# Kernel optimization log

Measured on AMD Instinct MI355X. Metric: run time of the kernel, lower is better.

The kernel has to match this reference:

```python
import jax, jax.numpy as jnp
import numpy as np


def setup_inputs() -> dict:
    key = jax.random.key(0)
    k1, k2 = jax.random.split(key)
    B, N, P = 8, 16384, 2048
    xyz = jax.random.uniform(k1, (B, N, 3), dtype=jnp.float32)
    center_xyz = jax.random.uniform(k2, (B, P, 3), dtype=jnp.float32)
    return {
        "xyz": xyz,
        "center_xyz": center_xyz,
        "max_radius": jnp.float32(0.2),
        "sample_num": 32,
    }


def reference(xyz, center_xyz, max_radius, sample_num):
    # xyz: [B, N, 3], center_xyz: [B, P, 3] -> idx: [B, P, sample_num] int32
    B, P, _ = center_xyz.shape
    N = xyz.shape[1]
    S = int(sample_num)

    # squared distances via ||c||^2 + ||x||^2 - 2 c.x (avoids [B,P,N,3] temp)
    xn = jnp.sum(xyz * xyz, axis=-1)                      # [B, N]
    cn = jnp.sum(center_xyz * center_xyz, axis=-1)        # [B, P]
    dot = jnp.einsum("bpd,bnd->bpn", center_xyz, xyz)     # [B, P, N]
    d2 = cn[:, :, None] + xn[:, None, :] - 2.0 * dot       # [B, P, N]

    mask = d2 < (max_radius * max_radius)                  # dist < r  <=>  dist^2 < r^2
    # rank of each point among the valid ones (in index order), as in torch.where order
    rank = jnp.cumsum(mask.astype(jnp.int32), axis=-1) - 1 # [B, P, N]
    take = mask & (rank < S)
    # valid points write into slot=rank; everything else into dump slot S (discarded)
    slot = jnp.where(take, rank, S)                        # [B, P, N]

    buf = jnp.zeros((B, P, S + 1), dtype=jnp.int32)        # zeros match torch init fill
    bi = jnp.arange(B)[:, None, None]
    pi = jnp.arange(P)[None, :, None]
    src = jnp.broadcast_to(jnp.arange(N, dtype=jnp.int32), (B, P, N))
    buf = buf.at[bi, pi, slot].set(src)
    return buf[:, :, :S]
```

## Files before the change

kernel.cpp:

```cpp
#include <hip/hip_runtime.h>
#include <hip/hip_bf16.h>


typedef float f32x4 __attribute__((ext_vector_type(4)));

__global__ __launch_bounds__(256) void pack_points(
    const float* __restrict__ xyz,
    f32x4* __restrict__ q,
    int total)
{
    const int n = blockIdx.x * blockDim.x + threadIdx.x;
    if (n >= total) return;
    const float x = xyz[(size_t)n * 3 + 0];
    const float y = xyz[(size_t)n * 3 + 1];
    const float z = xyz[(size_t)n * 3 + 2];
    const float xn = __builtin_fmaf(z, z,
                      __builtin_fmaf(y, y, __fmul_rn(x, x)));
    f32x4 v;
    v[0] = x; v[1] = y; v[2] = z; v[3] = xn;
    q[n] = v;
}

__global__ __launch_bounds__(64) void ball_query_wave4(
    const f32x4* __restrict__ q,
    const float* __restrict__ center,
    const float* __restrict__ p_radius,
    const int*   __restrict__ p_sample,
    int* __restrict__ out,
    int B, int N, int P)
{
    const int S = p_sample[0];
    const float r = p_radius[0];
    const float r2 = __fmul_rn(r, r);

    const int b = blockIdx.x & 7;
    const int g = blockIdx.x >> 3;
    const int c0 = b * P + g * 4;
    const int lane = threadIdx.x;

    float cx[4], cy[4], cz[4], cn[4];
    int cnt[4];
#pragma unroll
    for (int i = 0; i < 4; ++i) {
        const size_t c = (size_t)(c0 + i);
        cx[i] = center[c * 3 + 0];
        cy[i] = center[c * 3 + 1];
        cz[i] = center[c * 3 + 2];
        cn[i] = __builtin_fmaf(cz[i], cz[i],
                 __builtin_fmaf(cy[i], cy[i], __fmul_rn(cx[i], cx[i])));
        cnt[i] = 0;
    }

    const f32x4* qb = q + (size_t)b * N;
    int* ob = out + (size_t)c0 * S;

    for (int n0 = 0; n0 < N; n0 += 512) {
        if (cnt[0] >= S && cnt[1] >= S && cnt[2] >= S && cnt[3] >= S) break;

        f32x4 v[8];
#pragma unroll
        for (int j = 0; j < 8; ++j) {
            v[j] = qb[n0 + j * 64 + lane];
        }

#pragma unroll
        for (int i = 0; i < 4; ++i) {
            if (cnt[i] >= S) continue;
            int cc = cnt[i];
#pragma unroll
            for (int j = 0; j < 8; ++j) {
                const float x = v[j][0], y = v[j][1], z = v[j][2];
                const float xn = v[j][3];
                const float dot = __builtin_fmaf(cz[i], z,
                                   __builtin_fmaf(cy[i], y, __fmul_rn(cx[i], x)));
                const float d2 = __fsub_rn(__fadd_rn(cn[i], xn),
                                           __fmul_rn(2.0f, dot));

                const bool valid = d2 < r2;
                const unsigned long long m = __ballot(valid);
                const int rank = __builtin_amdgcn_mbcnt_hi(
                    (unsigned)(m >> 32),
                    __builtin_amdgcn_mbcnt_lo((unsigned)m, 0u));
                if (valid && (cc + rank) < S) {
                    ob[i * S + cc + rank] = n0 + j * 64 + lane;
                }
                cc += __popcll(m);
            }
            cnt[i] = cc;
        }
    }

#pragma unroll
    for (int i = 0; i < 4; ++i) {
        int c = cnt[i] > S ? S : cnt[i];
        for (int s = c + lane; s < S; s += 64) {
            ob[i * S + s] = 0;
        }
    }
}

extern "C" void kernel_launch(void* const* d_in, const int* in_sizes, int n_in,
                              void* d_out, int out_size, void* d_ws, size_t ws_size,
                              hipStream_t stream) {
    const float* xyz      = (const float*)d_in[0];
    const float* center   = (const float*)d_in[1];
    const float* p_radius = (const float*)d_in[2];
    const int*   p_sample = (const int*)d_in[3];

    const int B = 8;
    const int N = in_sizes[0] / (B * 3);
    const int P = in_sizes[1] / (B * 3);

    int* out = (int*)d_out;
    f32x4* q = (f32x4*)d_ws;

    const int total = B * N;
    pack_points<<<(total + 255) / 256, 256, 0, stream>>>(xyz, q, total);

    const int blocks = B * (P / 4);
    ball_query_wave4<<<blocks, 64, 0, stream>>>(
        q, center, p_radius, p_sample, out, B, N, P);
}
```

Measured before the change: 78.17 us.

## Use planar point layout with packed fp32 math and batched ballots

```diff
diff --git a/kernel.cpp b/kernel.cpp
--- a/kernel.cpp
+++ b/kernel.cpp
@@ -1,12 +1,35 @@
 #include <hip/hip_runtime.h>
-#include <hip/hip_bf16.h>
 
 
 typedef float f32x4 __attribute__((ext_vector_type(4)));
-
-__global__ __launch_bounds__(256) void pack_points(
+typedef float f32x2 __attribute__((ext_vector_type(2)));
+
+__device__ __forceinline__ f32x2 pk_mul(f32x2 a, f32x2 b) {
+    f32x2 d;
+    asm("v_pk_mul_f32 %0, %1, %2" : "=v"(d) : "v"(a), "v"(b));
+    return d;
+}
+__device__ __forceinline__ f32x2 pk_fma(f32x2 a, f32x2 b, f32x2 c) {
+    f32x2 d;
+    asm("v_pk_fma_f32 %0, %1, %2, %3" : "=v"(d) : "v"(a), "v"(b), "v"(c));
+    return d;
+}
+__device__ __forceinline__ f32x2 pk_add(f32x2 a, f32x2 b) {
+    f32x2 d;
+    asm("v_pk_add_f32 %0, %1, %2" : "=v"(d) : "v"(a), "v"(b));
+    return d;
+}
+__device__ __forceinline__ f32x2 pk_sub(f32x2 a, f32x2 b) {
+    f32x2 d;
+    asm("v_pk_add_f32 %0, %1, %2 neg_lo:[0,1] neg_hi:[0,1]"
+        : "=v"(d) : "v"(a), "v"(b));
+    return d;
+}
+
+__global__ __launch_bounds__(256) void pack_planes(
     const float* __restrict__ xyz,
-    f32x4* __restrict__ q,
+    float* __restrict__ qx, float* __restrict__ qy,
+    float* __restrict__ qz, float* __restrict__ qw,
     int total)
 {
     const int n = blockIdx.x * blockDim.x + threadIdx.x;
@@ -16,13 +39,67 @@
     const float z = xyz[(size_t)n * 3 + 2];
     const float xn = __builtin_fmaf(z, z,
                       __builtin_fmaf(y, y, __fmul_rn(x, x)));
-    f32x4 v;
-    v[0] = x; v[1] = y; v[2] = z; v[3] = xn;
-    q[n] = v;
-}
-
-__global__ __launch_bounds__(64) void ball_query_wave4(
-    const f32x4* __restrict__ q,
+    qx[n] = x; qy[n] = y; qz[n] = z; qw[n] = xn;
+}
+
+__device__ __forceinline__ int process_group(
+    f32x2 xlo, f32x2 xhi, f32x2 ylo, f32x2 yhi,
+    f32x2 zlo, f32x2 zhi, f32x2 wlo, f32x2 whi,
+    int vbase,
+    f32x2 pcx, f32x2 pcy, f32x2 pcz, f32x2 pcn, f32x2 p2,
+    int cc, int* __restrict__ obi, int S, float r2)
+{
+    f32x2 t0 = pk_mul(pcx, xlo);
+    t0 = pk_fma(pcy, ylo, t0);
+    t0 = pk_fma(pcz, zlo, t0);
+    f32x2 t1 = pk_mul(pcx, xhi);
+    t1 = pk_fma(pcy, yhi, t1);
+    t1 = pk_fma(pcz, zhi, t1);
+    f32x2 a0 = pk_add(pcn, wlo);
+    f32x2 a1 = pk_add(pcn, whi);
+    f32x2 b0 = pk_mul(p2, t0);
+    f32x2 b1 = pk_mul(p2, t1);
+    f32x2 d0 = pk_sub(a0, b0);
+    f32x2 d1 = pk_sub(a1, b1);
+
+    const bool v0 = d0[0] < r2;
+    const bool v1 = d0[1] < r2;
+    const bool v2 = d1[0] < r2;
+    const bool v3 = d1[1] < r2;
+    const unsigned long long m0 = __ballot(v0);
+    const unsigned long long m1 = __ballot(v1);
+    const unsigned long long m2 = __ballot(v2);
+    const unsigned long long m3 = __ballot(v3);
+
+    if ((m0 | m1 | m2 | m3) == 0ull) return cc;
+
+    int R = __builtin_amdgcn_mbcnt_lo((unsigned)m0, 0u);
+    R = __builtin_amdgcn_mbcnt_hi((unsigned)(m0 >> 32), R);
+    R = __builtin_amdgcn_mbcnt_lo((unsigned)m1, R);
+    R = __builtin_amdgcn_mbcnt_hi((unsigned)(m1 >> 32), R);
+    R = __builtin_amdgcn_mbcnt_lo((unsigned)m2, R);
+    R = __builtin_amdgcn_mbcnt_hi((unsigned)(m2 >> 32), R);
+    R = __builtin_amdgcn_mbcnt_lo((unsigned)m3, R);
+    R = __builtin_amdgcn_mbcnt_hi((unsigned)(m3 >> 32), R);
+
+    const int rank0 = R;
+    const int rank1 = rank0 + (v0 ? 1 : 0);
+    const int rank2 = rank1 + (v1 ? 1 : 0);
+    const int rank3 = rank2 + (v2 ? 1 : 0);
+
+    const int lim = S - cc;
+    if (v0 && rank0 < lim) obi[cc + rank0] = vbase + 0;
+    if (v1 && rank1 < lim) obi[cc + rank1] = vbase + 1;
+    if (v2 && rank2 < lim) obi[cc + rank2] = vbase + 2;
+    if (v3 && rank3 < lim) obi[cc + rank3] = vbase + 3;
+
+    cc += __popcll(m0) + __popcll(m1) + __popcll(m2) + __popcll(m3);
+    return cc;
+}
+
+__global__ __launch_bounds__(64) void ball_query_pk(
+    const float* __restrict__ qx, const float* __restrict__ qy,
+    const float* __restrict__ qz, const float* __restrict__ qw,
     const float* __restrict__ center,
     const float* __restrict__ p_radius,
     const int*   __restrict__ p_sample,
@@ -38,53 +115,64 @@
     const int c0 = b * P + g * 4;
     const int lane = threadIdx.x;
 
-    float cx[4], cy[4], cz[4], cn[4];
+    f32x2 pcx[4], pcy[4], pcz[4], pcn[4];
     int cnt[4];
 #pragma unroll
     for (int i = 0; i < 4; ++i) {
         const size_t c = (size_t)(c0 + i);
-        cx[i] = center[c * 3 + 0];
-        cy[i] = center[c * 3 + 1];
-        cz[i] = center[c * 3 + 2];
-        cn[i] = __builtin_fmaf(cz[i], cz[i],
-                 __builtin_fmaf(cy[i], cy[i], __fmul_rn(cx[i], cx[i])));
+        const float cx = center[c * 3 + 0];
+        const float cy = center[c * 3 + 1];
+        const float cz = center[c * 3 + 2];
+        const float cn = __builtin_fmaf(cz, cz,
+                          __builtin_fmaf(cy, cy, __fmul_rn(cx, cx)));
+        pcx[i][0] = cx; pcx[i][1] = cx;
+        pcy[i][0] = cy; pcy[i][1] = cy;
+        pcz[i][0] = cz; pcz[i][1] = cz;
+        pcn[i][0] = cn; pcn[i][1] = cn;
         cnt[i] = 0;
     }
-
-    const f32x4* qb = q + (size_t)b * N;
+    f32x2 p2; p2[0] = 2.0f; p2[1] = 2.0f;
+
+    const f32x4* X4 = (const f32x4*)(qx + (size_t)b * N);
+    const f32x4* Y4 = (const f32x4*)(qy + (size_t)b * N);
+    const f32x4* Z4 = (const f32x4*)(qz + (size_t)b * N);
+    const f32x4* W4 = (const f32x4*)(qw + (size_t)b * N);
     int* ob = out + (size_t)c0 * S;
 
     for (int n0 = 0; n0 < N; n0 += 512) {
         if (cnt[0] >= S && cnt[1] >= S && cnt[2] >= S && cnt[3] >= S) break;
 
-        f32x4 v[8];
-#pragma unroll
-        for (int j = 0; j < 8; ++j) {
-            v[j] = qb[n0 + j * 64 + lane];
-        }
+        const int i0 = (n0 >> 2) + lane;
+        const f32x4 xv0 = X4[i0],      yv0 = Y4[i0];
+        const f32x4 zv0 = Z4[i0],      wv0 = W4[i0];
+        const f32x4 xv1 = X4[i0 + 64], yv1 = Y4[i0 + 64];
+        const f32x4 zv1 = Z4[i0 + 64], wv1 = W4[i0 + 64];
+
+        f32x2 x0l, x0h, y0l, y0h, z0l, z0h, w0l, w0h;
+        f32x2 x1l, x1h, y1l, y1h, z1l, z1h, w1l, w1h;
+        x0l[0]=xv0[0]; x0l[1]=xv0[1]; x0h[0]=xv0[2]; x0h[1]=xv0[3];
+        y0l[0]=yv0[0]; y0l[1]=yv0[1]; y0h[0]=yv0[2]; y0h[1]=yv0[3];
+        z0l[0]=zv0[0]; z0l[1]=zv0[1]; z0h[0]=zv0[2]; z0h[1]=zv0[3];
+        w0l[0]=wv0[0]; w0l[1]=wv0[1]; w0h[0]=wv0[2]; w0h[1]=wv0[3];
+        x1l[0]=xv1[0]; x1l[1]=xv1[1]; x1h[0]=xv1[2]; x1h[1]=xv1[3];
+        y1l[0]=yv1[0]; y1l[1]=yv1[1]; y1h[0]=yv1[2]; y1h[1]=yv1[3];
+        z1l[0]=zv1[0]; z1l[1]=zv1[1]; z1h[0]=zv1[2]; z1h[1]=zv1[3];
+        w1l[0]=wv1[0]; w1l[1]=wv1[1]; w1h[0]=wv1[2]; w1h[1]=wv1[3];
+
+        const int vbase0 = n0 + 4 * lane;
+        const int vbase1 = vbase0 + 256;
 
 #pragma unroll
         for (int i = 0; i < 4; ++i) {
             if (cnt[i] >= S) continue;
             int cc = cnt[i];
-#pragma unroll
-            for (int j = 0; j < 8; ++j) {
-                const float x = v[j][0], y = v[j][1], z = v[j][2];
-                const float xn = v[j][3];
-                const float dot = __builtin_fmaf(cz[i], z,
-                                   __builtin_fmaf(cy[i], y, __fmul_rn(cx[i], x)));
-                const float d2 = __fsub_rn(__fadd_rn(cn[i], xn),
-                                           __fmul_rn(2.0f, dot));
-
-                const bool valid = d2 < r2;
-                const unsigned long long m = __ballot(valid);
-                const int rank = __builtin_amdgcn_mbcnt_hi(
-                    (unsigned)(m >> 32),
-                    __builtin_amdgcn_mbcnt_lo((unsigned)m, 0u));
-                if (valid && (cc + rank) < S) {
-                    ob[i * S + cc + rank] = n0 + j * 64 + lane;
-                }
-                cc += __popcll(m);
+            cc = process_group(x0l, x0h, y0l, y0h, z0l, z0h, w0l, w0h,
+                               vbase0, pcx[i], pcy[i], pcz[i], pcn[i], p2,
+                               cc, ob + i * S, S, r2);
+            if (cc < S) {
+                cc = process_group(x1l, x1h, y1l, y1h, z1l, z1h, w1l, w1h,
+                                   vbase1, pcx[i], pcy[i], pcz[i], pcn[i], p2,
+                                   cc, ob + i * S, S, r2);
             }
             cnt[i] = cc;
         }
@@ -112,12 +200,17 @@
     const int P = in_sizes[1] / (B * 3);
 
     int* out = (int*)d_out;
-    f32x4* q = (f32x4*)d_ws;
-
     const int total = B * N;
-    pack_points<<<(total + 255) / 256, 256, 0, stream>>>(xyz, q, total);
+
+    float* qx = (float*)d_ws;
+    float* qy = qx + total;
+    float* qz = qy + total;
+    float* qw = qz + total;
+
+    pack_planes<<<(total + 255) / 256, 256, 0, stream>>>(
+        xyz, qx, qy, qz, qw, total);
 
     const int blocks = B * (P / 4);
-    ball_query_wave4<<<blocks, 64, 0, stream>>>(
-        q, center, p_radius, p_sample, out, B, N, P);
-}
+    ball_query_pk<<<blocks, 64, 0, stream>>>(
+        qx, qy, qz, qw, center, p_radius, p_sample, out, B, N, P);
+}
```

Result: no change. 78.47 us (+0.4%).

## Fuse point packing into ball query and process four contiguous points per lane

Applied to the files above, without the earlier changes.

```diff
diff --git a/kernel.cpp b/kernel.cpp
--- a/kernel.cpp
+++ b/kernel.cpp
@@ -1,28 +1,67 @@
 #include <hip/hip_runtime.h>
-#include <hip/hip_bf16.h>
 
 
 typedef float f32x4 __attribute__((ext_vector_type(4)));
 
-__global__ __launch_bounds__(256) void pack_points(
-    const float* __restrict__ xyz,
-    f32x4* __restrict__ q,
-    int total)
+__device__ __forceinline__ int process_group(
+    float x0, float x1, float x2, float x3,
+    float y0, float y1, float y2, float y3,
+    float z0, float z1, float z2, float z3,
+    float w0, float w1, float w2, float w3,
+    int vbase,
+    float cx, float cy, float cz, float cn,
+    int cc, int* __restrict__ obi, int S, float r2)
 {
-    const int n = blockIdx.x * blockDim.x + threadIdx.x;
-    if (n >= total) return;
-    const float x = xyz[(size_t)n * 3 + 0];
-    const float y = xyz[(size_t)n * 3 + 1];
-    const float z = xyz[(size_t)n * 3 + 2];
-    const float xn = __builtin_fmaf(z, z,
-                      __builtin_fmaf(y, y, __fmul_rn(x, x)));
-    f32x4 v;
-    v[0] = x; v[1] = y; v[2] = z; v[3] = xn;
-    q[n] = v;
+    const float dot0 = __builtin_fmaf(cz, z0,
+                        __builtin_fmaf(cy, y0, __fmul_rn(cx, x0)));
+    const float dot1 = __builtin_fmaf(cz, z1,
+                        __builtin_fmaf(cy, y1, __fmul_rn(cx, x1)));
+    const float dot2 = __builtin_fmaf(cz, z2,
+                        __builtin_fmaf(cy, y2, __fmul_rn(cx, x2)));
+    const float dot3 = __builtin_fmaf(cz, z3,
+                        __builtin_fmaf(cy, y3, __fmul_rn(cx, x3)));
+    const float d20 = __fsub_rn(__fadd_rn(cn, w0), __fmul_rn(2.0f, dot0));
+    const float d21 = __fsub_rn(__fadd_rn(cn, w1), __fmul_rn(2.0f, dot1));
+    const float d22 = __fsub_rn(__fadd_rn(cn, w2), __fmul_rn(2.0f, dot2));
+    const float d23 = __fsub_rn(__fadd_rn(cn, w3), __fmul_rn(2.0f, dot3));
+
+    const bool v0 = d20 < r2;
+    const bool v1 = d21 < r2;
+    const bool v2 = d22 < r2;
+    const bool v3 = d23 < r2;
+    const unsigned long long m0 = __ballot(v0);
+    const unsigned long long m1 = __ballot(v1);
+    const unsigned long long m2 = __ballot(v2);
+    const unsigned long long m3 = __ballot(v3);
+
+    if ((m0 | m1 | m2 | m3) == 0ull) return cc;
+
+    int R = __builtin_amdgcn_mbcnt_lo((unsigned)m0, 0u);
+    R = __builtin_amdgcn_mbcnt_hi((unsigned)(m0 >> 32), R);
+    R = __builtin_amdgcn_mbcnt_lo((unsigned)m1, R);
+    R = __builtin_amdgcn_mbcnt_hi((unsigned)(m1 >> 32), R);
+    R = __builtin_amdgcn_mbcnt_lo((unsigned)m2, R);
+    R = __builtin_amdgcn_mbcnt_hi((unsigned)(m2 >> 32), R);
+    R = __builtin_amdgcn_mbcnt_lo((unsigned)m3, R);
+    R = __builtin_amdgcn_mbcnt_hi((unsigned)(m3 >> 32), R);
+
+    const int rank0 = R;
+    const int rank1 = rank0 + (v0 ? 1 : 0);
+    const int rank2 = rank1 + (v1 ? 1 : 0);
+    const int rank3 = rank2 + (v2 ? 1 : 0);
+
+    const int lim = S - cc;
+    if (v0 && rank0 < lim) obi[cc + rank0] = vbase + 0;
+    if (v1 && rank1 < lim) obi[cc + rank1] = vbase + 1;
+    if (v2 && rank2 < lim) obi[cc + rank2] = vbase + 2;
+    if (v3 && rank3 < lim) obi[cc + rank3] = vbase + 3;
+
+    cc += __popcll(m0) + __popcll(m1) + __popcll(m2) + __popcll(m3);
+    return cc;
 }
 
-__global__ __launch_bounds__(64) void ball_query_wave4(
-    const f32x4* __restrict__ q,
+__global__ __launch_bounds__(64) void ball_query_fused(
+    const float* __restrict__ xyz,
     const float* __restrict__ center,
     const float* __restrict__ p_radius,
     const int*   __restrict__ p_sample,
@@ -51,40 +90,66 @@
         cnt[i] = 0;
     }
 
-    const f32x4* qb = q + (size_t)b * N;
+    const f32x4* xb4 = (const f32x4*)(xyz + (size_t)b * N * 3);
     int* ob = out + (size_t)c0 * S;
 
     for (int n0 = 0; n0 < N; n0 += 512) {
         if (cnt[0] >= S && cnt[1] >= S && cnt[2] >= S && cnt[3] >= S) break;
 
-        f32x4 v[8];
-#pragma unroll
-        for (int j = 0; j < 8; ++j) {
-            v[j] = qb[n0 + j * 64 + lane];
-        }
+        const int qi0 = 3 * ((n0 >> 2) + lane);
+        const f32x4 a0 = xb4[qi0 + 0];
+        const f32x4 a1 = xb4[qi0 + 1];
+        const f32x4 a2 = xb4[qi0 + 2];
+        const f32x4 b0 = xb4[qi0 + 192];
+        const f32x4 b1 = xb4[qi0 + 193];
+        const f32x4 b2 = xb4[qi0 + 194];
+
+        const float gx0 = a0[0], gy0 = a0[1], gz0 = a0[2];
+        const float gx1 = a0[3], gy1 = a1[0], gz1 = a1[1];
+        const float gx2 = a1[2], gy2 = a1[3], gz2 = a2[0];
+        const float gx3 = a2[1], gy3 = a2[2], gz3 = a2[3];
+        const float hx0 = b0[0], hy0 = b0[1], hz0 = b0[2];
+        const float hx1 = b0[3], hy1 = b1[0], hz1 = b1[1];
+        const float hx2 = b1[2], hy2 = b1[3], hz2 = b2[0];
+        const float hx3 = b2[1], hy3 = b2[2], hz3 = b2[3];
+
+        const float gw0 = __builtin_fmaf(gz0, gz0,
+                           __builtin_fmaf(gy0, gy0, __fmul_rn(gx0, gx0)));
+        const float gw1 = __builtin_fmaf(gz1, gz1,
+                           __builtin_fmaf(gy1, gy1, __fmul_rn(gx1, gx1)));
+        const float gw2 = __builtin_fmaf(gz2, gz2,
+                           __builtin_fmaf(gy2, gy2, __fmul_rn(gx2, gx2)));
+        const float gw3 = __builtin_fmaf(gz3, gz3,
+                           __builtin_fmaf(gy3, gy3, __fmul_rn(gx3, gx3)));
+        const float hw0 = __builtin_fmaf(hz0, hz0,
+                           __builtin_fmaf(hy0, hy0, __fmul_rn(hx0, hx0)));
+        const float hw1 = __builtin_fmaf(hz1, hz1,
+                           __builtin_fmaf(hy1, hy1, __fmul_rn(hx1, hx1)));
+        const float hw2 = __builtin_fmaf(hz2, hz2,
+                           __builtin_fmaf(hy2, hy2, __fmul_rn(hx2, hx2)));
+        const float hw3 = __builtin_fmaf(hz3, hz3,
+                           __builtin_fmaf(hy3, hy3, __fmul_rn(hx3, hx3)));
+
+        const int vbase0 = n0 + 4 * lane;
+        const int vbase1 = vbase0 + 256;
 
 #pragma unroll
         for (int i = 0; i < 4; ++i) {
             if (cnt[i] >= S) continue;
             int cc = cnt[i];
-#pragma unroll
-            for (int j = 0; j < 8; ++j) {
-                const float x = v[j][0], y = v[j][1], z = v[j][2];
-                const float xn = v[j][3];
-                const float dot = __builtin_fmaf(cz[i], z,
-                                   __builtin_fmaf(cy[i], y, __fmul_rn(cx[i], x)));
-                const float d2 = __fsub_rn(__fadd_rn(cn[i], xn),
-                                           __fmul_rn(2.0f, dot));
-
-                const bool valid = d2 < r2;
-                const unsigned long long m = __ballot(valid);
-                const int rank = __builtin_amdgcn_mbcnt_hi(
-                    (unsigned)(m >> 32),
-                    __builtin_amdgcn_mbcnt_lo((unsigned)m, 0u));
-                if (valid && (cc + rank) < S) {
-                    ob[i * S + cc + rank] = n0 + j * 64 + lane;
-                }
-                cc += __popcll(m);
+            cc = process_group(gx0, gx1, gx2, gx3,
+                               gy0, gy1, gy2, gy3,
+                               gz0, gz1, gz2, gz3,
+                               gw0, gw1, gw2, gw3,
+                               vbase0, cx[i], cy[i], cz[i], cn[i],
+                               cc, ob + i * S, S, r2);
+            if (cc < S) {
+                cc = process_group(hx0, hx1, hx2, hx3,
+                                   hy0, hy1, hy2, hy3,
+                                   hz0, hz1, hz2, hz3,
+                                   hw0, hw1, hw2, hw3,
+                                   vbase1, cx[i], cy[i], cz[i], cn[i],
+                                   cc, ob + i * S, S, r2);
             }
             cnt[i] = cc;
         }
@@ -112,12 +177,9 @@
     const int P = in_sizes[1] / (B * 3);
 
     int* out = (int*)d_out;
-    f32x4* q = (f32x4*)d_ws;
-
-    const int total = B * N;
-    pack_points<<<(total + 255) / 256, 256, 0, stream>>>(xyz, q, total);
+    (void)d_ws; (void)ws_size;
 
     const int blocks = B * (P / 4);
-    ball_query_wave4<<<blocks, 64, 0, stream>>>(
-        q, center, p_radius, p_sample, out, B, N, P);
+    ball_query_fused<<<blocks, 64, 0, stream>>>(
+        xyz, center, p_radius, p_sample, out, B, N, P);
 }
```

Result: faster. 75.70 us (-3.2%).
